# Kernel tuning notes

Measured on AMD Instinct MI355X. Metric: run time of the kernel, lower is better.

Reference implementation:

```python
import jax, jax.numpy as jnp
import numpy as np

S = 8192  # sequence length
D = 256   # feature dim


def setup_inputs() -> dict:
    key = jax.random.key(0)
    kq, kk, kv = jax.random.split(key, 3)
    Q = jax.random.normal(kq, (S, D), dtype=jnp.float32)
    K = jax.random.normal(kk, (S, D), dtype=jnp.float32)
    V = jax.random.normal(kv, (S, D), dtype=jnp.float32)
    return {"Q": Q, "K": K, "V": V}


def reference(Q, K, V):
    # Faithful to the torch module: dk = K.size(-2) (the SEQUENCE length, not head dim)
    dk = K.shape[-2]
    scores = (Q @ K.T) / jnp.sqrt(jnp.float32(dk))  # [S, S]
    # F.softmax with implicit dim on a 2D tensor -> softmax over last dim (keys)
    attn = jax.nn.softmax(scores, axis=-1)
    return attn @ V  # [S, D]
```

## Files before the change

### kernel.cpp

```cpp
#include <hip/hip_runtime.h>


typedef __attribute__((ext_vector_type(4))) float    f32x4;
typedef __attribute__((ext_vector_type(4))) int      i32x4;
typedef __attribute__((ext_vector_type(4))) _Float16 h4;
typedef __attribute__((ext_vector_type(8))) _Float16 h8;
typedef long __attribute__((may_alias)) long_a;
typedef i32x4 __attribute__((may_alias)) i32x4_a;
typedef h8    __attribute__((may_alias)) h8_a;

#define SEQ 8192
#define DIM 256
#define NSPLIT 8
#define KPS (SEQ / NSPLIT)
#define BN 32
#define ITERS (KPS / BN)
#define BM 128

#define KSC (1.4426950408889634f / 90.50966799187808f)

__global__ void __launch_bounds__(256)
prep(const float* __restrict__ Q, const float* __restrict__ K,
     const float* __restrict__ V, unsigned char* __restrict__ Q8,
     unsigned char* __restrict__ K8, _Float16* __restrict__ Vt) {
    __shared__ _Float16 tile[32][264];
    int b = blockIdx.x, t = threadIdx.x;

    {
        int row = b * 32 + (t >> 3);
        int c0 = (t & 7) * 8;
        const f32x4* q4 = (const f32x4*)Q + (size_t)row * 64 + c0;
        const f32x4* k4 = (const f32x4*)K + (size_t)row * 64 + c0;
        int qo[8], ko[8];
        #pragma unroll
        for (int i = 0; i < 8; ++i) {
            f32x4 q = q4[i], k = k4[i];
            int dq = 0, dk = 0;
            dq = __builtin_amdgcn_cvt_pk_fp8_f32(q.x, q.y, dq, false);
            dq = __builtin_amdgcn_cvt_pk_fp8_f32(q.z, q.w, dq, true);
            dk = __builtin_amdgcn_cvt_pk_fp8_f32(k.x, k.y, dk, false);
            dk = __builtin_amdgcn_cvt_pk_fp8_f32(k.z, k.w, dk, true);
            qo[i] = dq; ko[i] = dk;
        }
        i32x4* qd = (i32x4*)(Q8 + (size_t)row * 256 + (t & 7) * 32);
        i32x4* kd = (i32x4*)(K8 + (size_t)row * 256 + (t & 7) * 32);
        qd[0] = *(i32x4*)&qo[0]; qd[1] = *(i32x4*)&qo[4];
        kd[0] = *(i32x4*)&ko[0]; kd[1] = *(i32x4*)&ko[4];
    }

    #pragma unroll
    for (int i = 0; i < 8; ++i) {
        int c = t + i * 256;
        int row = c >> 6, col = c & 63;
        f32x4 v = ((const f32x4*)V)[(size_t)(b * 32 + row) * 64 + col];
        tile[row][col * 4 + 0] = (_Float16)v.x;
        tile[row][col * 4 + 1] = (_Float16)v.y;
        tile[row][col * 4 + 2] = (_Float16)v.z;
        tile[row][col * 4 + 3] = (_Float16)v.w;
    }
    __syncthreads();
    _Float16* dst = Vt + (size_t)b * 8192 + t * 32;
    #pragma unroll
    for (int a = 0; a < 4; ++a) {
        h8 w;
        #pragma unroll
        for (int j = 0; j < 4; ++j) {
            w[j]     = tile[4 * a + j][t];
            w[4 + j] = tile[16 + 4 * a + j][t];
        }
        *(h8*)(dst + a * 8) = w;
    }
}

__global__ void __launch_bounds__(256, 2)
attn(const unsigned char* __restrict__ Q8, const unsigned char* __restrict__ K8,
     const _Float16* __restrict__ Vt, _Float16* __restrict__ Op,
     float* __restrict__ lp) {
    __shared__ unsigned char K_lds[2][32][272];
    __shared__ _Float16 V_lds[2][256][40];

    int tid = threadIdx.x;
    int wid = tid >> 6, lane = tid & 63;
    int l15 = lane & 15, qq = lane >> 4;
    int qt_blk = blockIdx.x >> 3, sp = blockIdx.x & 7;
    int qrow0 = qt_blk * BM + wid * 32;

    long qf[2][8];
    #pragma unroll
    for (int t = 0; t < 2; ++t) {
        const unsigned char* p = Q8 + (size_t)(qrow0 + t * 16 + l15) * DIM + qq * 8;
        #pragma unroll
        for (int s = 0; s < 8; ++s) qf[t][s] = *(const long_a*)(p + s * 32);
    }

    _Float16 one = (l15 == 0) ? (_Float16)1.0f : (_Float16)0.0f;
    h8 of = {one, one, one, one, one, one, one, one};

    const unsigned char* ksrc = K8 + (size_t)(sp * KPS + (tid >> 4)) * DIM + (tid & 15) * 16;
    const _Float16* vsrc = Vt + (size_t)sp * (KPS / BN) * 8192 + (tid >> 2) * 32 + (tid & 3) * 8;
    int kr = tid >> 4, kc = (tid & 15) * 16;
    int vr = tid >> 2, vc = (tid & 3) * 8;

    f32x4 acc[2][16] = {};
    f32x4 accl[2] = {};
    i32x4 kreg[2];
    h8 vreg[4];

    kreg[0] = *(const i32x4_a*)ksrc;
    kreg[1] = *(const i32x4_a*)(ksrc + 16 * DIM);
    #pragma unroll
    for (int p = 0; p < 4; ++p) vreg[p] = *(const h8_a*)(vsrc + p * 64 * 32);
    ksrc += BN * DIM; vsrc += 8192;
    *(i32x4_a*)&K_lds[0][kr][kc]      = kreg[0];
    *(i32x4_a*)&K_lds[0][kr + 16][kc] = kreg[1];
    #pragma unroll
    for (int p = 0; p < 4; ++p) *(h8_a*)&V_lds[0][vr + p * 64][vc] = vreg[p];
    __syncthreads();

    for (int it = 0; it < ITERS; ++it) {
        int b = it & 1;
        if (it + 1 < ITERS) {
            kreg[0] = *(const i32x4_a*)ksrc;
            kreg[1] = *(const i32x4_a*)(ksrc + 16 * DIM);
            #pragma unroll
            for (int p = 0; p < 4; ++p) vreg[p] = *(const h8_a*)(vsrc + p * 64 * 32);
            ksrc += BN * DIM; vsrc += 8192;
        }

        f32x4 sc[2][2] = {};
        #pragma unroll
        for (int s = 0; s < 8; ++s) {
            long kf0 = *(const long_a*)&K_lds[b][l15][s * 32 + qq * 8];
            long kf1 = *(const long_a*)&K_lds[b][16 + l15][s * 32 + qq * 8];
            #pragma unroll
            for (int t = 0; t < 2; ++t) {
                sc[0][t] = __builtin_amdgcn_mfma_f32_16x16x32_fp8_fp8(kf0, qf[t][s], sc[0][t], 0, 0, 0);
                sc[1][t] = __builtin_amdgcn_mfma_f32_16x16x32_fp8_fp8(kf1, qf[t][s], sc[1][t], 0, 0, 0);
            }
        }

        h8 pfrag[2];
        #pragma unroll
        for (int t = 0; t < 2; ++t)
            #pragma unroll
            for (int r = 0; r < 4; ++r) {
                pfrag[t][r]     = (_Float16)__builtin_amdgcn_exp2f(fminf(sc[0][t][r] * KSC, 16.0f));
                pfrag[t][4 + r] = (_Float16)__builtin_amdgcn_exp2f(fminf(sc[1][t][r] * KSC, 16.0f));
            }

        #pragma unroll
        for (int n = 0; n < 16; ++n) {
            h8 vf = *(const h8_a*)&V_lds[b][n * 16 + l15][qq * 8];
            acc[0][n] = __builtin_amdgcn_mfma_f32_16x16x32_f16(pfrag[0], vf, acc[0][n], 0, 0, 0);
            acc[1][n] = __builtin_amdgcn_mfma_f32_16x16x32_f16(pfrag[1], vf, acc[1][n], 0, 0, 0);
        }
        accl[0] = __builtin_amdgcn_mfma_f32_16x16x32_f16(pfrag[0], of, accl[0], 0, 0, 0);
        accl[1] = __builtin_amdgcn_mfma_f32_16x16x32_f16(pfrag[1], of, accl[1], 0, 0, 0);

        if (it + 1 < ITERS) {
            int nb = b ^ 1;
            *(i32x4_a*)&K_lds[nb][kr][kc]      = kreg[0];
            *(i32x4_a*)&K_lds[nb][kr + 16][kc] = kreg[1];
            #pragma unroll
            for (int p = 0; p < 4; ++p) *(h8_a*)&V_lds[nb][vr + p * 64][vc] = vreg[p];
            __syncthreads();
        }
    }

    #pragma unroll
    for (int t = 0; t < 2; ++t) {
        #pragma unroll
        for (int n = 0; n < 16; ++n)
            #pragma unroll
            for (int r = 0; r < 4; ++r) {
                int row = qrow0 + t * 16 + qq * 4 + r;
                Op[((size_t)sp * SEQ + row) * DIM + n * 16 + l15] = (_Float16)acc[t][n][r];
            }
        if (l15 == 0) {
            #pragma unroll
            for (int r = 0; r < 4; ++r)
                lp[(size_t)sp * SEQ + qrow0 + t * 16 + qq * 4 + r] = accl[t][r];
        }
    }
}

__global__ void combine(const _Float16* __restrict__ Op, const float* __restrict__ lp,
                        float* __restrict__ out) {
    int idx = blockIdx.x * 256 + threadIdx.x;
    int row = idx >> 6;
    f32x4 a = {};
    float l = 0.0f;
    #pragma unroll
    for (int s = 0; s < NSPLIT; ++s) {
        h4 h = *(const h4*)(Op + (size_t)s * SEQ * DIM + (size_t)idx * 4);
        a.x += (float)h.x; a.y += (float)h.y; a.z += (float)h.z; a.w += (float)h.w;
        l += lp[s * SEQ + row];
    }
    float linv = 1.0f / (l + 1e-20f);
    ((f32x4*)out)[idx] = a * linv;
}

extern "C" void kernel_launch(void* const* d_in, const int* in_sizes, int n_in,
                              void* d_out, int out_size, void* d_ws, size_t ws_size,
                              hipStream_t stream) {
    const float* Q = (const float*)d_in[0];
    const float* K = (const float*)d_in[1];
    const float* V = (const float*)d_in[2];
    float* out = (float*)d_out;

    char* ws = (char*)d_ws;
    unsigned char* Q8 = (unsigned char*)ws;
    unsigned char* K8 = (unsigned char*)(ws + (2u << 20));
    _Float16* Vt = (_Float16*)(ws + (4u << 20));
    _Float16* Op = (_Float16*)(ws + (8u << 20));
    float*    lp = (float*)(ws + (40u << 20));

    prep   <<<256, 256, 0, stream>>>(Q, K, V, Q8, K8, Vt);
    attn   <<<NSPLIT * (SEQ / BM), 256, 0, stream>>>(Q8, K8, Vt, Op, lp);
    combine<<<2048, 256, 0, stream>>>(Op, lp, out);
}
```

Before: 143.3 us.

## Drop LDS staging; load K/V fragments directly from pre-swizzled global layout

The prep kernel now writes K in an MFMA-fragment-ordered layout so each lane can load its K fragments straight from global memory. The attention kernel loses its LDS double buffering and barriers and reads K and V fragments directly from global (L2-cached). Blocks grow to 512 threads (8 waves, BM=256), so each block covers more query rows. The exp2 clamp is also removed. This trades LDS traffic and synchronisation for redundant per-wave global/L2 reads with no explicit prefetch, and drops the overflow guard on exp.

Result: slower. 197.1 us (+37.6%).

```diff
diff --git a/kernel.cpp b/kernel.cpp
--- a/kernel.cpp
+++ b/kernel.cpp
@@ -15,22 +15,22 @@
 #define KPS (SEQ / NSPLIT)
 #define BN 32
 #define ITERS (KPS / BN)
-#define BM 128
+#define BM 256
 
 #define KSC (1.4426950408889634f / 90.50966799187808f)
 
 __global__ void __launch_bounds__(256)
 prep(const float* __restrict__ Q, const float* __restrict__ K,
      const float* __restrict__ V, unsigned char* __restrict__ Q8,
-     unsigned char* __restrict__ K8, _Float16* __restrict__ Vt) {
+     unsigned char* __restrict__ K8f, _Float16* __restrict__ Vt) {
     __shared__ _Float16 tile[32][264];
     int b = blockIdx.x, t = threadIdx.x;
 
     {
         int row = b * 32 + (t >> 3);
-        int c0 = (t & 7) * 8;
-        const f32x4* q4 = (const f32x4*)Q + (size_t)row * 64 + c0;
-        const f32x4* k4 = (const f32x4*)K + (size_t)row * 64 + c0;
+        int s = t & 7;
+        const f32x4* q4 = (const f32x4*)Q + (size_t)row * 64 + s * 8;
+        const f32x4* k4 = (const f32x4*)K + (size_t)row * 64 + s * 8;
         int qo[8], ko[8];
         #pragma unroll
         for (int i = 0; i < 8; ++i) {
@@ -42,10 +42,15 @@
             dk = __builtin_amdgcn_cvt_pk_fp8_f32(k.z, k.w, dk, true);
             qo[i] = dq; ko[i] = dk;
         }
-        i32x4* qd = (i32x4*)(Q8 + (size_t)row * 256 + (t & 7) * 32);
-        i32x4* kd = (i32x4*)(K8 + (size_t)row * 256 + (t & 7) * 32);
+        i32x4* qd = (i32x4*)(Q8 + (size_t)row * 256 + s * 32);
         qd[0] = *(i32x4*)&qo[0]; qd[1] = *(i32x4*)&qo[4];
-        kd[0] = *(i32x4*)&ko[0]; kd[1] = *(i32x4*)&ko[4];
+
+        int kk = row & 31, sub = kk >> 4, l = kk & 15;
+        unsigned char* kb = K8f + (size_t)b * 8192 + sub * 4096
+                          + (s >> 1) * 1024 + (s & 1) * 8;
+        #pragma unroll
+        for (int q2 = 0; q2 < 4; ++q2)
+            *(long_a*)(kb + (q2 * 16 + l) * 16) = ((long*)ko)[q2];
     }
 
     #pragma unroll
@@ -72,13 +77,10 @@
     }
 }
 
-__global__ void __launch_bounds__(256, 2)
-attn(const unsigned char* __restrict__ Q8, const unsigned char* __restrict__ K8,
+__global__ void __launch_bounds__(512, 2)
+attn(const unsigned char* __restrict__ Q8, const unsigned char* __restrict__ K8f,
      const _Float16* __restrict__ Vt, _Float16* __restrict__ Op,
      float* __restrict__ lp) {
-    __shared__ unsigned char K_lds[2][32][272];
-    __shared__ _Float16 V_lds[2][256][40];
-
     int tid = threadIdx.x;
     int wid = tid >> 6, lane = tid & 63;
     int l15 = lane & 15, qq = lane >> 4;
@@ -96,42 +98,27 @@
     _Float16 one = (l15 == 0) ? (_Float16)1.0f : (_Float16)0.0f;
     h8 of = {one, one, one, one, one, one, one, one};
 
-    const unsigned char* ksrc = K8 + (size_t)(sp * KPS + (tid >> 4)) * DIM + (tid & 15) * 16;
-    const _Float16* vsrc = Vt + (size_t)sp * (KPS / BN) * 8192 + (tid >> 2) * 32 + (tid & 3) * 8;
-    int kr = tid >> 4, kc = (tid & 15) * 16;
-    int vr = tid >> 2, vc = (tid & 3) * 8;
+    const unsigned char* kbase = K8f + (size_t)(sp * (KPS / BN)) * 8192 + lane * 16;
+    const _Float16*      vbase = Vt  + (size_t)(sp * (KPS / BN)) * 4096 * 2
+                               + l15 * 32 + qq * 8;
 
     f32x4 acc[2][16] = {};
     f32x4 accl[2] = {};
-    i32x4 kreg[2];
-    h8 vreg[4];
-
-    kreg[0] = *(const i32x4_a*)ksrc;
-    kreg[1] = *(const i32x4_a*)(ksrc + 16 * DIM);
-    #pragma unroll
-    for (int p = 0; p < 4; ++p) vreg[p] = *(const h8_a*)(vsrc + p * 64 * 32);
-    ksrc += BN * DIM; vsrc += 8192;
-    *(i32x4_a*)&K_lds[0][kr][kc]      = kreg[0];
-    *(i32x4_a*)&K_lds[0][kr + 16][kc] = kreg[1];
-    #pragma unroll
-    for (int p = 0; p < 4; ++p) *(h8_a*)&V_lds[0][vr + p * 64][vc] = vreg[p];
-    __syncthreads();
 
     for (int it = 0; it < ITERS; ++it) {
-        int b = it & 1;
-        if (it + 1 < ITERS) {
-            kreg[0] = *(const i32x4_a*)ksrc;
-            kreg[1] = *(const i32x4_a*)(ksrc + 16 * DIM);
-            #pragma unroll
-            for (int p = 0; p < 4; ++p) vreg[p] = *(const h8_a*)(vsrc + p * 64 * 32);
-            ksrc += BN * DIM; vsrc += 8192;
-        }
+        const unsigned char* kt = kbase + it * 8192;
+        union { i32x4 v; long l[2]; } kfr[2][4];
+        #pragma unroll
+        for (int sub = 0; sub < 2; ++sub)
+            #pragma unroll
+            for (int p = 0; p < 4; ++p)
+                kfr[sub][p].v = *(const i32x4_a*)(kt + sub * 4096 + p * 1024);
 
         f32x4 sc[2][2] = {};
         #pragma unroll
         for (int s = 0; s < 8; ++s) {
-            long kf0 = *(const long_a*)&K_lds[b][l15][s * 32 + qq * 8];
-            long kf1 = *(const long_a*)&K_lds[b][16 + l15][s * 32 + qq * 8];
+            long kf0 = kfr[0][s >> 1].l[s & 1];
+            long kf1 = kfr[1][s >> 1].l[s & 1];
             #pragma unroll
             for (int t = 0; t < 2; ++t) {
                 sc[0][t] = __builtin_amdgcn_mfma_f32_16x16x32_fp8_fp8(kf0, qf[t][s], sc[0][t], 0, 0, 0);
@@ -144,27 +131,19 @@
         for (int t = 0; t < 2; ++t)
             #pragma unroll
             for (int r = 0; r < 4; ++r) {
-                pfrag[t][r]     = (_Float16)__builtin_amdgcn_exp2f(fminf(sc[0][t][r] * KSC, 16.0f));
-                pfrag[t][4 + r] = (_Float16)__builtin_amdgcn_exp2f(fminf(sc[1][t][r] * KSC, 16.0f));
+                pfrag[t][r]     = (_Float16)__builtin_amdgcn_exp2f(sc[0][t][r] * KSC);
+                pfrag[t][4 + r] = (_Float16)__builtin_amdgcn_exp2f(sc[1][t][r] * KSC);
             }
 
+        const _Float16* vt = vbase + it * 8192;
         #pragma unroll
         for (int n = 0; n < 16; ++n) {
-            h8 vf = *(const h8_a*)&V_lds[b][n * 16 + l15][qq * 8];
+            h8 vf = *(const h8_a*)(vt + n * 512);
             acc[0][n] = __builtin_amdgcn_mfma_f32_16x16x32_f16(pfrag[0], vf, acc[0][n], 0, 0, 0);
             acc[1][n] = __builtin_amdgcn_mfma_f32_16x16x32_f16(pfrag[1], vf, acc[1][n], 0, 0, 0);
         }
         accl[0] = __builtin_amdgcn_mfma_f32_16x16x32_f16(pfrag[0], of, accl[0], 0, 0, 0);
         accl[1] = __builtin_amdgcn_mfma_f32_16x16x32_f16(pfrag[1], of, accl[1], 0, 0, 0);
-
-        if (it + 1 < ITERS) {
-            int nb = b ^ 1;
-            *(i32x4_a*)&K_lds[nb][kr][kc]      = kreg[0];
-            *(i32x4_a*)&K_lds[nb][kr + 16][kc] = kreg[1];
-            #pragma unroll
-            for (int p = 0; p < 4; ++p) *(h8_a*)&V_lds[nb][vr + p * 64][vc] = vreg[p];
-            __syncthreads();
-        }
     }
 
     #pragma unroll
@@ -209,13 +188,13 @@
     float* out = (float*)d_out;
 
     char* ws = (char*)d_ws;
-    unsigned char* Q8 = (unsigned char*)ws;
-    unsigned char* K8 = (unsigned char*)(ws + (2u << 20));
+    unsigned char* Q8  = (unsigned char*)ws;
+    unsigned char* K8f = (unsigned char*)(ws + (2u << 20));
     _Float16* Vt = (_Float16*)(ws + (4u << 20));
     _Float16* Op = (_Float16*)(ws + (8u << 20));
     float*    lp = (float*)(ws + (40u << 20));
 
-    prep   <<<256, 256, 0, stream>>>(Q, K, V, Q8, K8, Vt);
-    attn   <<<NSPLIT * (SEQ / BM), 256, 0, stream>>>(Q8, K8, Vt, Op, lp);
+    prep   <<<256, 256, 0, stream>>>(Q, K, V, Q8, K8f, Vt);
+    attn   <<<NSPLIT * (SEQ / BM), 512, 0, stream>>>(Q8, K8f, Vt, Op, lp);
     combine<<<2048, 256, 0, stream>>>(Op, lp, out);
 }
```
